# Kernel optimization log

Measured on AMD Instinct MI355X. Metric: run time of the kernel, lower is better.

Reference implementation:

```python
import jax, jax.numpy as jnp
import numpy as np

B, S, D = 4, 1024, 1024
NS = 8            # n_samples
NT = 10           # n_steps
EXP_NOISE = 0.1
STEP = 0.01
TEMP = 1.0
LN_EPS = 1e-5


def _ln(x, g, b):
    m = jnp.mean(x, axis=-1, keepdims=True)
    v = jnp.mean(jnp.square(x - m), axis=-1, keepdims=True)
    return (x - m) * jax.lax.rsqrt(v + LN_EPS) * g + b


def setup_inputs() -> dict:
    key = jax.random.key(0)
    ks = jax.random.split(key, 8)
    sc = 0.02
    return {
        "hidden": jax.random.normal(ks[0], (B, S, D), jnp.float32),
        "W1": jax.random.normal(ks[1], (D, 2 * D), jnp.float32) * sc,
        "b1": jnp.zeros((2 * D,), jnp.float32),
        "ln1_g": jnp.ones((2 * D,), jnp.float32),
        "ln1_b": jnp.zeros((2 * D,), jnp.float32),
        "W2": jax.random.normal(ks[2], (2 * D, D), jnp.float32) * sc,
        "b2": jnp.zeros((D,), jnp.float32),
        "Ew1": jax.random.normal(ks[3], (2 * D, D), jnp.float32) * sc,
        "Eb1": jnp.zeros((D,), jnp.float32),
        "Eln_g": jnp.ones((D,), jnp.float32),
        "Eln_b": jnp.zeros((D,), jnp.float32),
        "Ew2": jax.random.normal(ks[4], (D, D // 2), jnp.float32) * sc,
        "Eb2": jnp.zeros((D // 2,), jnp.float32),
        "Ew3": jax.random.normal(ks[5], (D // 2, 1), jnp.float32) * sc,
        "Eb3": jnp.zeros((1,), jnp.float32),
    }


def reference(hidden, W1, b1, ln1_g, ln1_b, W2, b2,
              Ew1, Eb1, Eln_g, Eln_b, Ew2, Eb2, Ew3, Eb3):
    # context: per-seq mean, identical at every position (keepdim+expand in torch)
    ctx = jnp.mean(hidden, axis=1)                      # [B, D]
    # context_predictor (result is .detach()-ed inside pcn_refine)
    cp = jax.nn.relu(_ln(ctx @ W1 + b1, ln1_g, ln1_b)) @ W2 + b2   # [B, D]
    cp = jax.lax.stop_gradient(cp)

    nkey = jax.random.key(42)
    # n_samples exploration hypotheses: hidden + N(0, exploration_noise)
    expl = jax.random.normal(jax.random.fold_in(nkey, 0), (NS, B, S, D), hidden.dtype)
    hyp = hidden[None] + expl * EXP_NOISE               # [NS, B, S, D]

    cpb = cp[None, :, None, :]                          # broadcast to [NS,B,S,D]

    # PCN refinement: linear pull toward cp + small noise on all but last step
    def step_fn(cur, t):
        cur = cur - STEP * (cur - cpb)
        noise = jax.random.normal(jax.random.fold_in(nkey, t + 1), cur.shape, cur.dtype)
        cur = cur + noise * 0.01 * (t < NT - 1)
        return cur, None

    hyp, _ = jax.lax.scan(step_fn, hyp, jnp.arange(NT))

    # energy_net on concat([latent, context]): split first linear to avoid concat
    Ew1_h, Ew1_c = Ew1[:D], Ew1[D:]
    ce = ctx @ Ew1_c + Eb1                              # context contribution [B, D]
    e = hyp @ Ew1_h + ce[None, :, None, :]              # [NS, B, S, D]
    e = jax.nn.relu(_ln(e, Eln_g, Eln_b))
    e = jax.nn.relu(e @ Ew2 + Eb2)                      # [NS, B, S, D//2]
    e = (e @ Ew3 + Eb3)[..., 0]                         # [NS, B, S]
    energies = jnp.mean(e, axis=2)                      # [NS, B]

    probs = jax.nn.softmax(-energies / TEMP, axis=0)    # [NS, B]
    selected = jnp.einsum('nb,nbsd->bsd', probs, hyp)   # [B, S, D]
    return selected
```

## Files before the change

### kernel.cpp

```cpp
#include <hip/hip_runtime.h>
#include <hip/hip_bf16.h>
#include <stdint.h>
#include <math.h>


#define NS_ 8
#define B_ 4
#define S_ 1024
#define D_ 1024
#define NROWS (NS_*B_*S_)
#define NELEM (1u<<25)

typedef __attribute__((ext_vector_type(8))) short short8;
typedef __attribute__((ext_vector_type(4))) float f32x4;

struct RngParams {
  uint32_t k0[10], k1[10];
  float coef[10];
  float aH, aCP;
};

__host__ __device__ __forceinline__ uint32_t rotl32_(uint32_t x, int r) {
#if defined(__HIP_DEVICE_COMPILE__)
  return __builtin_rotateleft32(x, (uint32_t)r);
#else
  return (x << r) | (x >> (32 - r));
#endif
}

__host__ __device__ __forceinline__ void tf2x32(uint32_t k0, uint32_t k1,
                                                uint32_t x0, uint32_t x1,
                                                uint32_t &o0, uint32_t &o1) {
  uint32_t k2 = k0 ^ k1 ^ 0x1BD11BDAu;
  x0 += k0; x1 += k1;
  x0 += x1; x1 = rotl32_(x1, 13); x1 ^= x0;
  x0 += x1; x1 = rotl32_(x1, 15); x1 ^= x0;
  x0 += x1; x1 = rotl32_(x1, 26); x1 ^= x0;
  x0 += x1; x1 = rotl32_(x1, 6);  x1 ^= x0;
  x0 += k1; x1 += k2 + 1u;
  x0 += x1; x1 = rotl32_(x1, 17); x1 ^= x0;
  x0 += x1; x1 = rotl32_(x1, 29); x1 ^= x0;
  x0 += x1; x1 = rotl32_(x1, 16); x1 ^= x0;
  x0 += x1; x1 = rotl32_(x1, 24); x1 ^= x0;
  x0 += k2; x1 += k0 + 2u;
  x0 += x1; x1 = rotl32_(x1, 13); x1 ^= x0;
  x0 += x1; x1 = rotl32_(x1, 15); x1 ^= x0;
  x0 += x1; x1 = rotl32_(x1, 26); x1 ^= x0;
  x0 += x1; x1 = rotl32_(x1, 6);  x1 ^= x0;
  x0 += k0; x1 += k1 + 3u;
  x0 += x1; x1 = rotl32_(x1, 17); x1 ^= x0;
  x0 += x1; x1 = rotl32_(x1, 29); x1 ^= x0;
  x0 += x1; x1 = rotl32_(x1, 16); x1 ^= x0;
  x0 += x1; x1 = rotl32_(x1, 24); x1 ^= x0;
  x0 += k1; x1 += k2 + 4u;
  x0 += x1; x1 = rotl32_(x1, 13); x1 ^= x0;
  x0 += x1; x1 = rotl32_(x1, 15); x1 ^= x0;
  x0 += x1; x1 = rotl32_(x1, 26); x1 ^= x0;
  x0 += x1; x1 = rotl32_(x1, 6);  x1 ^= x0;
  x0 += k2; x1 += k0 + 5u;
  o0 = x0; o1 = x1;
}

__device__ __forceinline__ float b2n_scaled(uint32_t bits) {
  const float lo = -0.99999994f;
  float f = __uint_as_float((bits >> 9) | 0x3f800000u);
  float x = fmaxf(lo, fmaf(f, 2.0f, lo - 2.0f));
  float t = fmaf(-x, x, 1.0f);
  float l2 = __log2f(t);
  float p;
  if (l2 > -7.2134752f) {
    float v = fmaf(l2, -1.0f, -3.6067376f);
    p = 2.11766e-09f;
    p = fmaf(p, v, 3.73196e-08f);
    p = fmaf(p, v, -5.52622e-07f);
    p = fmaf(p, v, -9.93683e-07f);
    p = fmaf(p, v, 7.13556e-05f);
    p = fmaf(p, v, -5.90466e-04f);
    p = fmaf(p, v, -2.83857e-03f);
    p = fmaf(p, v, 2.41772e-01f);
    p = fmaf(p, v, 2.1233136f);
  } else {
    float s = sqrtf(l2 * -0.69314718f) - 3.0f;
    p = -2.83146e-04f;
    p = fmaf(p, s, 1.42766e-04f);
    p = fmaf(p, s, 1.90826e-03f);
    p = fmaf(p, s, -5.19503e-03f);
    p = fmaf(p, s, 8.11695e-03f);
    p = fmaf(p, s, -1.07799e-02f);
    p = fmaf(p, s, 1.33486e-02f);
    p = fmaf(p, s, 1.41658104f);
    p = fmaf(p, s, 4.00643763f);
  }
  return p * x;
}

__device__ __forceinline__ float noise10(const RngParams& P, uint32_t i) {
  float acc = 0.f;
  #pragma unroll
  for (int j = 0; j < 10; ++j) {
    uint32_t w0, w1;
    tf2x32(P.k0[j], P.k1[j], 0u, i, w0, w1);
    acc = fmaf(P.coef[j], b2n_scaled(w0 ^ w1), acc);
  }
  return acc;
}

__device__ __forceinline__ uint16_t bf16u(float x) {
  __hip_bfloat16 h = __float2bfloat16(x);
  return *(uint16_t*)&h;
}
__device__ __forceinline__ float bf2f(uint32_t u) {
  return __uint_as_float(u << 16);
}

__device__ void wcvt_body(const float* __restrict__ src, uint16_t* __restrict__ dst,
                          int K, int N, int bx, int by) {
  __shared__ float tile[64][65];
  int n0 = bx * 64, k0 = by * 64;
  int tid = threadIdx.x;
  #pragma unroll
  for (int i = 0; i < 16; ++i) {
    int lin = tid + i * 256;
    int tr = lin >> 6, tc = lin & 63;
    tile[tr][tc] = src[(size_t)(k0 + tr) * N + n0 + tc];
  }
  __syncthreads();
  #pragma unroll
  for (int i = 0; i < 8; ++i) {
    int lin = tid + i * 256;
    int tr = lin >> 5, tc2 = (lin & 31) * 2;
    uint32_t pk = (uint32_t)bf16u(tile[tc2][tr]) | ((uint32_t)bf16u(tile[tc2 + 1][tr]) << 16);
    *(uint32_t*)(&dst[(size_t)(n0 + tr) * K + k0 + tc2]) = pk;
  }
}

__global__ void k_prep(const float* __restrict__ Ew1, const float* __restrict__ Ew2,
                       const float* __restrict__ hidden,
                       uint16_t* __restrict__ WT1, uint16_t* __restrict__ WT2,
                       float* __restrict__ part) {
  int bi = blockIdx.x;
  if (bi < 256) {
    wcvt_body(Ew1, WT1, 1024, 1024, bi & 15, bi >> 4);
  } else if (bi < 384) {
    int j = bi - 256;
    wcvt_body(Ew2, WT2, 1024, 512, j & 7, j >> 3);
  } else {
    int cb = bi - 384;
    int b = cb >> 6, ch = cb & 63;
    const float* p = hidden + (size_t)b * (S_ * D_) + (size_t)ch * 16 * 1024;
    int tid = threadIdx.x;
    #pragma unroll
    for (int k = 0; k < 4; ++k) {
      int d = tid + k * 256;
      float s = 0.f;
      #pragma unroll
      for (int t = 0; t < 16; ++t) s += p[t * 1024 + d];
      part[(size_t)cb * 1024 + d] = s;
    }
  }
}

__global__ void k_ctxB(const float* __restrict__ part, float* __restrict__ ctx) {
  int idx = blockIdx.x * 256 + threadIdx.x;
  int b = idx >> 10, d = idx & 1023;
  float s = 0.f;
  #pragma unroll 8
  for (int c = 0; c < 64; ++c) s += part[((size_t)(b * 64 + c)) * 1024 + d];
  ctx[idx] = s * (1.0f / 1024.0f);
}

__global__ void k_fc1(const float* __restrict__ ctx, const float* __restrict__ W1,
                      const float* __restrict__ b1, float* __restrict__ t1) {
  __shared__ float red[4][64];
  int b = blockIdx.x >> 5;
  int j0 = (blockIdx.x & 31) * 64;
  int l = threadIdx.x & 63, w = threadIdx.x >> 6;
  int j = j0 + l;
  const float* c = ctx + b * 1024 + w * 256;
  const float* wp = W1 + (size_t)(w * 256) * 2048 + j;
  float s = 0.f;
  #pragma unroll 8
  for (int k = 0; k < 256; ++k) s += c[k] * wp[(size_t)k * 2048];
  red[w][l] = s; __syncthreads();
  if (w == 0)
    t1[b * 2048 + j] = red[0][l] + red[1][l] + red[2][l] + red[3][l] + b1[j];
}

__global__ void k_ln_relu(float* __restrict__ t1, const float* __restrict__ g,
                          const float* __restrict__ bb) {
  __shared__ float red[256];
  int row = blockIdx.x, tid = threadIdx.x;
  float* x = t1 + row * 2048;
  float v[8];
  #pragma unroll
  for (int q = 0; q < 8; ++q) v[q] = x[tid + q * 256];
  float s = 0.f;
  #pragma unroll
  for (int q = 0; q < 8; ++q) s += v[q];
  red[tid] = s; __syncthreads();
  for (int off = 128; off > 0; off >>= 1) { if (tid < off) red[tid] += red[tid + off]; __syncthreads(); }
  float m = red[0] * (1.0f / 2048.0f);
  __syncthreads();
  float s2 = 0.f;
  #pragma unroll
  for (int q = 0; q < 8; ++q) { float d = v[q] - m; s2 += d * d; }
  red[tid] = s2; __syncthreads();
  for (int off = 128; off > 0; off >>= 1) { if (tid < off) red[tid] += red[tid + off]; __syncthreads(); }
  float var = red[0] * (1.0f / 2048.0f);
  float rs = 1.0f / sqrtf(var + 1e-5f);
  #pragma unroll
  for (int q = 0; q < 8; ++q) {
    int j = tid + q * 256;
    float z = (v[q] - m) * rs * g[j] + bb[j];
    x[j] = fmaxf(z, 0.0f);
  }
}

__global__ void k_fc2(const float* __restrict__ t1, const float* __restrict__ W2,
                      const float* __restrict__ b2, const float* __restrict__ ctx,
                      const float* __restrict__ Ew1c, const float* __restrict__ Eb1,
                      float* __restrict__ cp, float* __restrict__ ce) {
  __shared__ float red[4][64];
  int b = blockIdx.x >> 4;
  int j0 = (blockIdx.x & 15) * 64;
  int l = threadIdx.x & 63, w = threadIdx.x >> 6;
  int j = j0 + l;
  float s = 0.f;
  if (blockIdx.y == 0) {
    const float* a = t1 + b * 2048 + w * 512;
    const float* wp = W2 + (size_t)(w * 512) * 1024 + j;
    #pragma unroll 8
    for (int k = 0; k < 512; ++k) s += a[k] * wp[(size_t)k * 1024];
  } else {
    const float* a = ctx + b * 1024 + w * 256;
    const float* wp = Ew1c + (size_t)(w * 256) * 1024 + j;
    #pragma unroll 8
    for (int k = 0; k < 256; ++k) s += a[k] * wp[(size_t)k * 1024];
  }
  red[w][l] = s; __syncthreads();
  if (w == 0) {
    float r = red[0][l] + red[1][l] + red[2][l] + red[3][l];
    if (blockIdx.y == 0) cp[b * 1024 + j] = r + b2[j];
    else                 ce[b * 1024 + j] = r + Eb1[j];
  }
}

#define ZP_OF   0
#define RED2_OF 32768
#define STM_OF  33280
#define STR_OF  33344
#define RED_OF  33408
#define APAN_OF 33664

__device__ __forceinline__ int pswz(int row, int byteInRow) {
  return (row * 2048 + byteInRow) ^ ((row & 7) << 4);
}

template<bool BIG>
__global__ __launch_bounds__(256, 4) void k_fused(
    const float* __restrict__ hidden, const float* __restrict__ cp,
    const float* __restrict__ ce, uint32_t* __restrict__ hypPairs,
    const uint16_t* __restrict__ WT1, const uint16_t* __restrict__ WT2,
    const float* __restrict__ Eln_g, const float* __restrict__ Eln_b,
    const float* __restrict__ Eb2, const float* __restrict__ Ew3,
    float* __restrict__ erows, RngParams P)
{
  __shared__ __align__(16) char smem[BIG ? 33664 : 66432];
  const int tid = threadIdx.x;
  const int lane = tid & 63;
  const int w = tid >> 6;
  const int rl = lane & 15;
  const int kg = lane >> 4;
  const int r0 = blockIdx.x * 16;
  const int bidx = (r0 >> 10) & 3;
  float* rowm = (float*)(smem + STM_OF);
  float* rowr = (float*)(smem + STR_OF);
  float* red  = (float*)(smem + RED_OF);
  float* red2 = (float*)(smem + RED2_OF);

  #pragma unroll 2
  for (int q = 0; q < 32; ++q) {
    int p = tid + q * 256;
    int row = p >> 9, c0 = (p & 511) * 2;
    uint32_t i0 = (uint32_t)(r0 + row) * 1024u + (uint32_t)c0;
    float nz0 = noise10(P, i0);
    float nz1 = noise10(P, i0 + 1u);
    float2 hv = *(const float2*)(hidden + (i0 & 0x3FFFFFu));
    float2 cv = *(const float2*)(cp + (bidx << 10) + c0);
    float h0 = fmaf(P.aH, hv.x, fmaf(P.aCP, cv.x, nz0));
    float h1 = fmaf(P.aH, hv.y, fmaf(P.aCP, cv.y, nz1));
    uint32_t pk = (uint32_t)bf16u(h0) | ((uint32_t)bf16u(h1) << 16);
    if (BIG) hypPairs[i0 >> 1] = pk;
    else *(uint32_t*)(smem + APAN_OF + pswz(row, c0 * 2)) = pk;
  }
  __syncthreads();

  float s1a[4] = {0.f, 0.f, 0.f, 0.f};
  float s2a[4] = {0.f, 0.f, 0.f, 0.f};
  const uint16_t* Abase = (const uint16_t*)hypPairs + (size_t)(r0 + rl) * 1024 + kg * 8;
  for (int g = 0; g < 4; ++g) {
    f32x4 acc[4] = {};
    const uint16_t* b0 = WT1 + (size_t)(g * 256 + w * 64 +  0 + rl) * 1024 + kg * 8;
    const uint16_t* b1p = WT1 + (size_t)(g * 256 + w * 64 + 16 + rl) * 1024 + kg * 8;
    const uint16_t* b2p = WT1 + (size_t)(g * 256 + w * 64 + 32 + rl) * 1024 + kg * 8;
    const uint16_t* b3p = WT1 + (size_t)(g * 256 + w * 64 + 48 + rl) * 1024 + kg * 8;
    #pragma unroll 8
    for (int kt = 0; kt < 32; ++kt) {
      short8 af;
      if (BIG) af = *(const short8*)(Abase + kt * 32);
      else     af = *(const short8*)(smem + APAN_OF + pswz(rl, kt * 64 + kg * 16));
      short8 f0 = *(const short8*)(b0  + kt * 32);
      short8 f1 = *(const short8*)(b1p + kt * 32);
      short8 f2 = *(const short8*)(b2p + kt * 32);
      short8 f3 = *(const short8*)(b3p + kt * 32);
      acc[0] = __builtin_amdgcn_mfma_f32_16x16x32_bf16(af, f0, acc[0], 0, 0, 0);
      acc[1] = __builtin_amdgcn_mfma_f32_16x16x32_bf16(af, f1, acc[1], 0, 0, 0);
      acc[2] = __builtin_amdgcn_mfma_f32_16x16x32_bf16(af, f2, acc[2], 0, 0, 0);
      acc[3] = __builtin_amdgcn_mfma_f32_16x16x32_bf16(af, f3, acc[3], 0, 0, 0);
    }
    #pragma unroll
    for (int j = 0; j < 4; ++j) {
      int C = g * 256 + w * 64 + j * 16 + rl;
      float cev = ce[(bidx << 10) + C];
      #pragma unroll
      for (int i = 0; i < 4; ++i) {
        float y = acc[j][i] + cev;
        s1a[i] += y;
        s2a[i] = fmaf(y, y, s2a[i]);
        *(uint16_t*)(smem + ZP_OF + pswz(kg * 4 + i, C * 2)) = bf16u(y);
      }
    }
  }
  #pragma unroll
  for (int i = 0; i < 4; ++i) {
    #pragma unroll
    for (int m = 1; m < 16; m <<= 1) {
      s1a[i] += __shfl_xor(s1a[i], m);
      s2a[i] += __shfl_xor(s2a[i], m);
    }
  }
  if (rl == 0) {
    #pragma unroll
    for (int i = 0; i < 4; ++i) {
      red2[(w * 16 + kg * 4 + i) * 2 + 0] = s1a[i];
      red2[(w * 16 + kg * 4 + i) * 2 + 1] = s2a[i];
    }
  }
  __syncthreads();

  if (tid < 16) {
    float s1 = 0.f, s2 = 0.f;
    #pragma unroll
    for (int wv = 0; wv < 4; ++wv) {
      s1 += red2[(wv * 16 + tid) * 2 + 0];
      s2 += red2[(wv * 16 + tid) * 2 + 1];
    }
    float m = s1 * (1.0f / 1024.0f);
    float var = fmaxf(s2 * (1.0f / 1024.0f) - m * m, 0.0f);
    rowm[tid] = m;
    rowr[tid] = 1.0f / sqrtf(var + 1e-5f);
  }
  __syncthreads();

  for (int q = 0; q < 64; ++q) {
    int e = tid + q * 256;
    int row = e >> 10, col = e & 1023;
    uint16_t* zp = (uint16_t*)(smem + ZP_OF + pswz(row, col * 2));
    float v = bf2f(*zp);
    float z = (v - rowm[row]) * rowr[row] * Eln_g[col] + Eln_b[col];
    *zp = bf16u(fmaxf(z, 0.f));
  }
  __syncthreads();

  float ep0 = 0.f, ep1 = 0.f, ep2 = 0.f, ep3 = 0.f;
  for (int g = 0; g < 2; ++g) {
    f32x4 acc[4] = {};
    const uint16_t* b0 = WT2 + (size_t)(g * 256 + w * 64 +  0 + rl) * 1024 + kg * 8;
    const uint16_t* b1p = WT2 + (size_t)(g * 256 + w * 64 + 16 + rl) * 1024 + kg * 8;
    const uint16_t* b2p = WT2 + (size_t)(g * 256 + w * 64 + 32 + rl) * 1024 + kg * 8;
    const uint16_t* b3p = WT2 + (size_t)(g * 256 + w * 64 + 48 + rl) * 1024 + kg * 8;
    #pragma unroll 8
    for (int kt = 0; kt < 32; ++kt) {
      short8 af = *(const short8*)(smem + ZP_OF + pswz(rl, kt * 64 + kg * 16));
      short8 f0 = *(const short8*)(b0  + kt * 32);
      short8 f1 = *(const short8*)(b1p + kt * 32);
      short8 f2 = *(const short8*)(b2p + kt * 32);
      short8 f3 = *(const short8*)(b3p + kt * 32);
      acc[0] = __builtin_amdgcn_mfma_f32_16x16x32_bf16(af, f0, acc[0], 0, 0, 0);
      acc[1] = __builtin_amdgcn_mfma_f32_16x16x32_bf16(af, f1, acc[1], 0, 0, 0);
      acc[2] = __builtin_amdgcn_mfma_f32_16x16x32_bf16(af, f2, acc[2], 0, 0, 0);
      acc[3] = __builtin_amdgcn_mfma_f32_16x16x32_bf16(af, f3, acc[3], 0, 0, 0);
    }
    #pragma unroll
    for (int j = 0; j < 4; ++j) {
      int C = g * 256 + w * 64 + j * 16 + rl;
      float eb = Eb2[C], w3 = Ew3[C];
      ep0 = fmaf(fmaxf(acc[j][0] + eb, 0.f), w3, ep0);
      ep1 = fmaf(fmaxf(acc[j][1] + eb, 0.f), w3, ep1);
      ep2 = fmaf(fmaxf(acc[j][2] + eb, 0.f), w3, ep2);
      ep3 = fmaf(fmaxf(acc[j][3] + eb, 0.f), w3, ep3);
    }
  }
  #pragma unroll
  for (int m = 1; m < 16; m <<= 1) {
    ep0 += __shfl_xor(ep0, m);
    ep1 += __shfl_xor(ep1, m);
    ep2 += __shfl_xor(ep2, m);
    ep3 += __shfl_xor(ep3, m);
  }
  if (rl == 0) {
    red[w * 16 + kg * 4 + 0] = ep0;
    red[w * 16 + kg * 4 + 1] = ep1;
    red[w * 16 + kg * 4 + 2] = ep2;
    red[w * 16 + kg * 4 + 3] = ep3;
  }
  __syncthreads();
  if (tid < 16)
    erows[r0 + tid] = red[tid] + red[16 + tid] + red[32 + tid] + red[48 + tid];
}

__global__ void k_energy(const float* __restrict__ erows, const float* __restrict__ Eb3,
                         float* __restrict__ energ) {
  __shared__ float red[256];
  int nb = blockIdx.x, tid = threadIdx.x;
  const float* x = erows + nb * 1024;
  float s = x[tid] + x[tid + 256] + x[tid + 512] + x[tid + 768];
  red[tid] = s; __syncthreads();
  for (int off = 128; off > 0; off >>= 1) { if (tid < off) red[tid] += red[tid + off]; __syncthreads(); }
  if (tid == 0) energ[nb] = red[0] * (1.0f / 1024.0f) + Eb3[0];
}

template<bool BIG>
__global__ __launch_bounds__(256) void k_select(
    const float* __restrict__ hidden, const float* __restrict__ cp,
    const float* __restrict__ energ, const uint32_t* __restrict__ hypPairs,
    float* __restrict__ out, RngParams P)
{
  uint32_t pe = blockIdx.x * 256u + threadIdx.x;
  uint32_t i0 = pe * 2u;
  uint32_t b = (i0 >> 20) & 3u;
  float e[8];
  #pragma unroll
  for (int n = 0; n < 8; ++n) e[n] = -energ[n * 4 + b];
  float mx = e[0];
  #pragma unroll
  for (int n = 1; n < 8; ++n) mx = fmaxf(mx, e[n]);
  float p[8]; float s = 0.f;
  #pragma unroll
  for (int n = 0; n < 8; ++n) { p[n] = expf(e[n] - mx); s += p[n]; }
  float inv = 1.0f / s;
  float a0 = 0.f, a1 = 0.f;
  if (BIG) {
    #pragma unroll
    for (int n = 0; n < 8; ++n) {
      uint32_t pk = hypPairs[pe + ((uint32_t)n << 21)];
      a0 = fmaf(p[n], __uint_as_float(pk << 16), a0);
      a1 = fmaf(p[n], __uint_as_float(pk & 0xffff0000u), a1);
    }
    *(float2*)(out + i0) = make_float2(a0 * inv, a1 * inv);
  } else {
    float2 hv = *(const float2*)(hidden + i0);
    float2 cv = *(const float2*)(cp + ((b << 10) | (i0 & 1023u)));
    #pragma unroll
    for (int n = 0; n < 8; ++n) {
      a0 = fmaf(p[n], noise10(P, i0 + ((uint32_t)n << 22)), a0);
      a1 = fmaf(p[n], noise10(P, i0 + 1u + ((uint32_t)n << 22)), a1);
    }
    float o0 = fmaf(P.aH, hv.x, P.aCP * cv.x) + a0 * inv;
    float o1 = fmaf(P.aH, hv.y, P.aCP * cv.y) + a1 * inv;
    *(float2*)(out + i0) = make_float2(o0, o1);
  }
}

extern "C" void kernel_launch(void* const* d_in, const int* in_sizes, int n_in,
                              void* d_out, int out_size, void* d_ws, size_t ws_size,
                              hipStream_t stream) {
  const float* hidden = (const float*)d_in[0];
  const float* W1    = (const float*)d_in[1];
  const float* b1    = (const float*)d_in[2];
  const float* ln1_g = (const float*)d_in[3];
  const float* ln1_b = (const float*)d_in[4];
  const float* W2    = (const float*)d_in[5];
  const float* b2    = (const float*)d_in[6];
  const float* Ew1   = (const float*)d_in[7];
  const float* Eb1   = (const float*)d_in[8];
  const float* Eln_g = (const float*)d_in[9];
  const float* Eln_b = (const float*)d_in[10];
  const float* Ew2   = (const float*)d_in[11];
  const float* Eb2   = (const float*)d_in[12];
  const float* Ew3   = (const float*)d_in[13];
  const float* Eb3   = (const float*)d_in[14];
  float* out = (float*)d_out;

  const size_t HYP_B  = (size_t)NELEM * 2;
  const size_t WT1_B  = 1024ull * 1024 * 2;
  const size_t WT2_B  = 512ull * 1024 * 2;
  const size_t PART_B = 256ull * 1024 * 4;
  const size_t SMALL_B = (4096 + 8192 + 4096 + 4096 + 32768 + 32) * 4;
  bool big = ws_size >= HYP_B + WT1_B + WT2_B + PART_B + SMALL_B + 1024;

  char* ws = (char*)d_ws;
  uint32_t* hypPairs = nullptr;
  size_t off = 0;
  if (big) { hypPairs = (uint32_t*)ws; off += HYP_B; }
  uint16_t* WT1 = (uint16_t*)(ws + off); off += WT1_B;
  uint16_t* WT2 = (uint16_t*)(ws + off); off += WT2_B;
  float* part  = (float*)(ws + off);     off += PART_B;
  float* ctx   = (float*)(ws + off);
  float* t1    = ctx + 4096;
  float* cp    = t1 + 8192;
  float* ce    = cp + 4096;
  float* erows = ce + 4096;
  float* energ = erows + 32768;

  RngParams P;
  for (uint32_t t = 0; t < 10; ++t) {
    uint32_t o0, o1;
    tf2x32(0u, 42u, 0u, t, o0, o1);
    P.k0[t] = o0; P.k1[t] = o1;
  }
  double a = pow(0.99, 10);
  P.coef[0] = (float)(0.1 * a);
  for (int j = 1; j <= 9; ++j) P.coef[j] = (float)(0.01 * pow(0.99, 10 - j));
  P.aH = (float)a;
  P.aCP = (float)(1.0 - a);

  k_prep<<<640, 256, 0, stream>>>(Ew1, Ew2, hidden, WT1, WT2, part);
  k_ctxB<<<16, 256, 0, stream>>>(part, ctx);
  k_fc1<<<128, 256, 0, stream>>>(ctx, W1, b1, t1);
  k_ln_relu<<<4, 256, 0, stream>>>(t1, ln1_g, ln1_b);
  k_fc2<<<dim3(64, 2), 256, 0, stream>>>(t1, W2, b2, ctx, Ew1 + (size_t)1024 * 1024, Eb1, cp, ce);
  if (big)
    k_fused<true><<<2048, 256, 0, stream>>>(hidden, cp, ce, hypPairs, WT1, WT2,
                                            Eln_g, Eln_b, Eb2, Ew3, erows, P);
  else
    k_fused<false><<<2048, 256, 0, stream>>>(hidden, cp, ce, (uint32_t*)ws, WT1, WT2,
                                             Eln_g, Eln_b, Eb2, Ew3, erows, P);
  k_energy<<<32, 256, 0, stream>>>(erows, Eb3, energ);
  if (big)
    k_select<true><<<8192, 256, 0, stream>>>(hidden, cp, energ, hypPairs, out, P);
  else
    k_select<false><<<8192, 256, 0, stream>>>(hidden, cp, energ, nullptr, out, P);
}
```

Baseline: 1.045 ms.

## Move fused-kernel reduction scratch to global memory to raise occupancy

Shrinks the fused kernel's LDS footprint to exactly 32KB by moving the per-block row-stat and energy reduction scratch into a global workspace buffer, and raises the launch-bounds occupancy hint (5 for the big path). It also interleaves two Threefry streams per loop iteration with partial unrolling, hoists the cp loads out of the noise loop, and restructures the LayerNorm pass so gamma/beta stay in registers across rows. The aim is more resident blocks per CU and less register pressure. The cost is that reductions now go through global memory with __syncthreads-only ordering, which adds latency and relies on intra-block global visibility.

```diff
diff --git a/kernel.cpp b/kernel.cpp
--- a/kernel.cpp
+++ b/kernel.cpp
@@ -94,9 +94,24 @@
   return p * x;
 }
 
+__device__ __forceinline__ void noise10x2(const RngParams& P, uint32_t i0,
+                                          float& n0, float& n1) {
+  float a0 = 0.f, a1 = 0.f;
+  #pragma unroll 2
+  for (int j = 0; j < 10; ++j) {
+    uint32_t w0, w1, v0, v1;
+    tf2x32(P.k0[j], P.k1[j], 0u, i0, w0, w1);
+    tf2x32(P.k0[j], P.k1[j], 0u, i0 + 1u, v0, v1);
+    float c = P.coef[j];
+    a0 = fmaf(c, b2n_scaled(w0 ^ w1), a0);
+    a1 = fmaf(c, b2n_scaled(v0 ^ v1), a1);
+  }
+  n0 = a0; n1 = a1;
+}
+
 __device__ __forceinline__ float noise10(const RngParams& P, uint32_t i) {
   float acc = 0.f;
-  #pragma unroll
+  #pragma unroll 2
   for (int j = 0; j < 10; ++j) {
     uint32_t w0, w1;
     tf2x32(P.k0[j], P.k1[j], 0u, i, w0, w1);
@@ -246,26 +261,22 @@
 }
 
 #define ZP_OF   0
-#define RED2_OF 32768
-#define STM_OF  33280
-#define STR_OF  33344
-#define RED_OF  33408
-#define APAN_OF 33664
+#define APAN_OF 32768
 
 __device__ __forceinline__ int pswz(int row, int byteInRow) {
   return (row * 2048 + byteInRow) ^ ((row & 7) << 4);
 }
 
 template<bool BIG>
-__global__ __launch_bounds__(256, 4) void k_fused(
+__global__ __launch_bounds__(256, BIG ? 5 : 2) void k_fused(
     const float* __restrict__ hidden, const float* __restrict__ cp,
     const float* __restrict__ ce, uint32_t* __restrict__ hypPairs,
     const uint16_t* __restrict__ WT1, const uint16_t* __restrict__ WT2,
     const float* __restrict__ Eln_g, const float* __restrict__ Eln_b,
     const float* __restrict__ Eb2, const float* __restrict__ Ew3,
-    float* __restrict__ erows, RngParams P)
+    float* __restrict__ erows, float* __restrict__ bscr, RngParams P)
 {
-  __shared__ __align__(16) char smem[BIG ? 33664 : 66432];
+  __shared__ __align__(16) char smem[BIG ? 32768 : 65536];
   const int tid = threadIdx.x;
   const int lane = tid & 63;
   const int w = tid >> 6;
@@ -273,20 +284,20 @@
   const int kg = lane >> 4;
   const int r0 = blockIdx.x * 16;
   const int bidx = (r0 >> 10) & 3;
-  float* rowm = (float*)(smem + STM_OF);
-  float* rowr = (float*)(smem + STR_OF);
-  float* red  = (float*)(smem + RED_OF);
-  float* red2 = (float*)(smem + RED2_OF);
-
-  #pragma unroll 2
+  float* bs = bscr + (size_t)blockIdx.x * 256;
+
+  const float2* cp2 = (const float2*)(cp + (bidx << 10));
+  const float2 cvA = cp2[tid];
+  const float2 cvB = cp2[tid + 256];
+  #pragma unroll 1
   for (int q = 0; q < 32; ++q) {
     int p = tid + q * 256;
     int row = p >> 9, c0 = (p & 511) * 2;
     uint32_t i0 = (uint32_t)(r0 + row) * 1024u + (uint32_t)c0;
-    float nz0 = noise10(P, i0);
-    float nz1 = noise10(P, i0 + 1u);
+    float nz0, nz1;
+    noise10x2(P, i0, nz0, nz1);
     float2 hv = *(const float2*)(hidden + (i0 & 0x3FFFFFu));
-    float2 cv = *(const float2*)(cp + (bidx << 10) + c0);
+    float2 cv = (q & 1) ? cvB : cvA;
     float h0 = fmaf(P.aH, hv.x, fmaf(P.aCP, cv.x, nz0));
     float h1 = fmaf(P.aH, hv.y, fmaf(P.aCP, cv.y, nz1));
     uint32_t pk = (uint32_t)bf16u(h0) | ((uint32_t)bf16u(h1) << 16);
@@ -342,8 +353,8 @@
   if (rl == 0) {
     #pragma unroll
     for (int i = 0; i < 4; ++i) {
-      red2[(w * 16 + kg * 4 + i) * 2 + 0] = s1a[i];
-      red2[(w * 16 + kg * 4 + i) * 2 + 1] = s2a[i];
+      bs[(w * 16 + kg * 4 + i) * 2 + 0] = s1a[i];
+      bs[(w * 16 + kg * 4 + i) * 2 + 1] = s2a[i];
     }
   }
   __syncthreads();
@@ -352,23 +363,35 @@
     float s1 = 0.f, s2 = 0.f;
     #pragma unroll
     for (int wv = 0; wv < 4; ++wv) {
-      s1 += red2[(wv * 16 + tid) * 2 + 0];
-      s2 += red2[(wv * 16 + tid) * 2 + 1];
+      s1 += bs[(wv * 16 + tid) * 2 + 0];
+      s2 += bs[(wv * 16 + tid) * 2 + 1];
     }
     float m = s1 * (1.0f / 1024.0f);
     float var = fmaxf(s2 * (1.0f / 1024.0f) - m * m, 0.0f);
-    rowm[tid] = m;
-    rowr[tid] = 1.0f / sqrtf(var + 1e-5f);
-  }
-  __syncthreads();
-
-  for (int q = 0; q < 64; ++q) {
-    int e = tid + q * 256;
-    int row = e >> 10, col = e & 1023;
-    uint16_t* zp = (uint16_t*)(smem + ZP_OF + pswz(row, col * 2));
-    float v = bf2f(*zp);
-    float z = (v - rowm[row]) * rowr[row] * Eln_g[col] + Eln_b[col];
-    *zp = bf16u(fmaxf(z, 0.f));
+    bs[128 + tid] = m;
+    bs[144 + tid] = 1.0f / sqrtf(var + 1e-5f);
+  }
+  __syncthreads();
+
+  {
+    float gv[4], bv[4];
+    #pragma unroll
+    for (int qq = 0; qq < 4; ++qq) {
+      gv[qq] = Eln_g[tid + qq * 256];
+      bv[qq] = Eln_b[tid + qq * 256];
+    }
+    #pragma unroll 1
+    for (int row = 0; row < 16; ++row) {
+      float m = bs[128 + row], rs = bs[144 + row];
+      #pragma unroll
+      for (int qq = 0; qq < 4; ++qq) {
+        int col = tid + qq * 256;
+        uint16_t* zp = (uint16_t*)(smem + ZP_OF + pswz(row, col * 2));
+        float v = bf2f(*zp);
+        float z = fmaf((v - m) * rs, gv[qq], bv[qq]);
+        *zp = bf16u(fmaxf(z, 0.f));
+      }
+    }
   }
   __syncthreads();
 
@@ -409,14 +432,14 @@
     ep3 += __shfl_xor(ep3, m);
   }
   if (rl == 0) {
-    red[w * 16 + kg * 4 + 0] = ep0;
-    red[w * 16 + kg * 4 + 1] = ep1;
-    red[w * 16 + kg * 4 + 2] = ep2;
-    red[w * 16 + kg * 4 + 3] = ep3;
+    bs[192 + w * 16 + kg * 4 + 0] = ep0;
+    bs[192 + w * 16 + kg * 4 + 1] = ep1;
+    bs[192 + w * 16 + kg * 4 + 2] = ep2;
+    bs[192 + w * 16 + kg * 4 + 3] = ep3;
   }
   __syncthreads();
   if (tid < 16)
-    erows[r0 + tid] = red[tid] + red[16 + tid] + red[32 + tid] + red[48 + tid];
+    erows[r0 + tid] = bs[192 + tid] + bs[208 + tid] + bs[224 + tid] + bs[240 + tid];
 }
 
 __global__ void k_energy(const float* __restrict__ erows, const float* __restrict__ Eb3,
@@ -496,8 +519,9 @@
   const size_t WT1_B  = 1024ull * 1024 * 2;
   const size_t WT2_B  = 512ull * 1024 * 2;
   const size_t PART_B = 256ull * 1024 * 4;
+  const size_t BSCR_B = 2048ull * 256 * 4;
   const size_t SMALL_B = (4096 + 8192 + 4096 + 4096 + 32768 + 32) * 4;
-  bool big = ws_size >= HYP_B + WT1_B + WT2_B + PART_B + SMALL_B + 1024;
+  bool big = ws_size >= HYP_B + WT1_B + WT2_B + PART_B + BSCR_B + SMALL_B + 1024;
 
   char* ws = (char*)d_ws;
   uint32_t* hypPairs = nullptr;
@@ -506,6 +530,7 @@
   uint16_t* WT1 = (uint16_t*)(ws + off); off += WT1_B;
   uint16_t* WT2 = (uint16_t*)(ws + off); off += WT2_B;
   float* part  = (float*)(ws + off);     off += PART_B;
+  float* bscr  = (float*)(ws + off);     off += BSCR_B;
   float* ctx   = (float*)(ws + off);
   float* t1    = ctx + 4096;
   float* cp    = t1 + 8192;
@@ -532,10 +557,10 @@
   k_fc2<<<dim3(64, 2), 256, 0, stream>>>(t1, W2, b2, ctx, Ew1 + (size_t)1024 * 1024, Eb1, cp, ce);
   if (big)
     k_fused<true><<<2048, 256, 0, stream>>>(hidden, cp, ce, hypPairs, WT1, WT2,
-                                            Eln_g, Eln_b, Eb2, Ew3, erows, P);
+                                            Eln_g, Eln_b, Eb2, Ew3, erows, bscr, P);
   else
     k_fused<false><<<2048, 256, 0, stream>>>(hidden, cp, ce, (uint32_t*)ws, WT1, WT2,
-                                             Eln_g, Eln_b, Eb2, Ew3, erows, P);
+                                             Eln_g, Eln_b, Eb2, Ew3, erows, bscr, P);
   k_energy<<<32, 256, 0, stream>>>(erows, Eb3, energ);
   if (big)
     k_select<true><<<8192, 256, 0, stream>>>(hidden, cp, energ, hypPairs, out, P);
```

Result: slower. 1.073 ms (+2.6%).
